# Optimization experiments

Measured on AMD Instinct MI355X. Metric: run time of the kernel, lower is better.

The kernel has to match this reference:

```python
import jax, jax.numpy as jnp
import numpy as np

EPS = 1e-5
INV_SQRT2 = 0.7071067811865476

def _rmsnorm(x, w):
    rms = jnp.sqrt(jnp.sum(x * x, axis=-1) / x.shape[-1] + EPS)
    return x / rms[..., None] * w

def _gelu(x):
    # exact erf-based GELU as in the torch module
    return x * (1.0 + jax.scipy.special.erf(x * INV_SQRT2)) * 0.5

def setup_inputs() -> dict:
    key = jax.random.key(0)
    ks = jax.random.split(key, 8)
    B, S, D, DFF = 4, 2048, 1024, 4096
    s = 0.02  # realistic init scale keeps softmax non-degenerate
    return {
        "x": jax.random.normal(ks[0], (B, S, D), jnp.float32),
        "ln1": jax.random.uniform(ks[1], (D,), jnp.float32),
        "ln2": jax.random.uniform(ks[2], (D,), jnp.float32),
        "ffn1": jax.random.normal(ks[3], (DFF, D), jnp.float32) * s,
        "ffn2": jax.random.normal(ks[4], (D, DFF), jnp.float32) * s,
        "k_proj": jax.random.normal(ks[5], (D, D), jnp.float32) * s,
        "q_proj": jax.random.normal(ks[6], (D, D), jnp.float32) * s,
        "v_proj": jax.random.normal(ks[7], (D, D), jnp.float32) * s,
        "out_proj": jax.random.normal(jax.random.fold_in(key, 99), (D, D), jnp.float32) * s,
    }

def reference(x, ln1, ln2, ffn1, ffn2, k_proj, q_proj, v_proj, out_proj):
    S = x.shape[1]
    d_k = x.shape[-1]
    # --- attention branch (single-head, as in source) ---
    h = _rmsnorm(x, ln1)
    Q = h @ q_proj.T  # [B,S,D]
    K = h @ k_proj.T
    V = h @ v_proj.T
    scores = jnp.einsum('bqd,bkd->bqk', Q, K) / jnp.sqrt(jnp.float32(d_k))
    attn = jax.nn.softmax(scores, axis=-1)
    # source: softmax first, then zero out strict-upper (future) entries, renormalize
    causal = jnp.tril(jnp.ones((S, S), jnp.float32))
    attn = attn * causal
    attn = attn / jnp.sum(attn, axis=-1, keepdims=True)
    mh = jnp.einsum('bqk,bkd->bqd', attn, V) @ out_proj
    y = x + mh
    # --- FFN branch: NOTE source feeds RMSNorm2(x), not y ---
    h2 = _rmsnorm(x, ln2)
    ff = _gelu(h2 @ ffn1.T) @ ffn2.T
    return y + ff
```

## Files before the change

kernel.cpp:

```cpp
#include <hip/hip_runtime.h>
#include <math.h>

typedef __bf16 bf16_t;
typedef __bf16 bf16x8 __attribute__((ext_vector_type(8)));
typedef float f32x4 __attribute__((ext_vector_type(4)));

#define LDS16(g, l) __builtin_amdgcn_global_load_lds( \
    (__attribute__((address_space(1))) void*)(g),     \
    (__attribute__((address_space(3))) void*)(l), 16, 0, 0)

__global__ __launch_bounds__(256) void prep_kernel(
    const float* __restrict__ qp, const float* __restrict__ kp,
    const float* __restrict__ vp, const float* __restrict__ f1,
    const float* __restrict__ f2, const float* __restrict__ op,
    const float* __restrict__ x, const float* __restrict__ ln1,
    bf16_t* __restrict__ qkvb, bf16_t* __restrict__ f1b,
    bf16_t* __restrict__ f2b, bf16_t* __restrict__ opT,
    bf16_t* __restrict__ h1)
{
    __shared__ float tile[32][33];
    __shared__ float red[4];
    int bid = blockIdx.x;
    int t = threadIdx.x;
    if (bid < 11264) {
        size_t i = ((size_t)bid * 256 + t) * 4;
        const float* src;
        bf16_t* dst;
        if (i < 3145728) {
            if (i < 1048576)      { src = qp + i;             dst = qkvb + i; }
            else if (i < 2097152) { src = kp + (i - 1048576); dst = qkvb + i; }
            else                  { src = vp + (i - 2097152); dst = qkvb + i; }
        } else if (i < 7340032) { src = f1 + (i - 3145728); dst = f1b + (i - 3145728); }
        else                    { src = f2 + (i - 7340032); dst = f2b + (i - 7340032); }
        float4 v = *(const float4*)src;
        dst[0] = (bf16_t)v.x; dst[1] = (bf16_t)v.y;
        dst[2] = (bf16_t)v.z; dst[3] = (bf16_t)v.w;
    } else if (bid < 12288) {
        int b2 = bid - 11264;
        int c0 = (b2 & 31) * 32, r0 = (b2 >> 5) * 32;
        int tx = t & 31, ty = t >> 5;
#pragma unroll
        for (int i = 0; i < 32; i += 8)
            tile[ty + i][tx] = op[(size_t)(r0 + ty + i) * 1024 + c0 + tx];
        __syncthreads();
#pragma unroll
        for (int i = 0; i < 32; i += 8)
            opT[(size_t)(c0 + ty + i) * 1024 + r0 + tx] = (bf16_t)tile[tx][ty + i];
    } else {
        int row = bid - 12288;
        float4 xv = ((const float4*)(x + (size_t)row * 1024))[t];
        float ss = xv.x * xv.x + xv.y * xv.y + xv.z * xv.z + xv.w * xv.w;
#pragma unroll
        for (int o = 32; o > 0; o >>= 1) ss += __shfl_xor(ss, o, 64);
        if ((t & 63) == 0) red[t >> 6] = ss;
        __syncthreads();
        ss = red[0] + red[1] + red[2] + red[3];
        float rinv = rsqrtf(ss * (1.0f / 1024.0f) + 1e-5f);
        float4 wv = ((const float4*)ln1)[t];
        bf16_t* hp = h1 + (size_t)row * 1024 + t * 4;
        hp[0] = (bf16_t)(xv.x * rinv * wv.x);
        hp[1] = (bf16_t)(xv.y * rinv * wv.y);
        hp[2] = (bf16_t)(xv.z * rinv * wv.z);
        hp[3] = (bf16_t)(xv.w * rinv * wv.w);
    }
}

__global__ __launch_bounds__(256) void rmsnorm_kernel(
    const float* __restrict__ x, const float* __restrict__ w,
    bf16_t* __restrict__ h)
{
    int row = blockIdx.x;
    int t = threadIdx.x;
    float4 xv = ((const float4*)(x + (size_t)row * 1024))[t];
    float ss = xv.x * xv.x + xv.y * xv.y + xv.z * xv.z + xv.w * xv.w;
#pragma unroll
    for (int o = 32; o > 0; o >>= 1) ss += __shfl_xor(ss, o, 64);
    __shared__ float red[4];
    if ((t & 63) == 0) red[t >> 6] = ss;
    __syncthreads();
    ss = red[0] + red[1] + red[2] + red[3];
    float rinv = rsqrtf(ss * (1.0f / 1024.0f) + 1e-5f);
    float4 wv = ((const float4*)w)[t];
    bf16_t* hp = h + (size_t)row * 1024 + t * 4;
    hp[0] = (bf16_t)(xv.x * rinv * wv.x);
    hp[1] = (bf16_t)(xv.y * rinv * wv.y);
    hp[2] = (bf16_t)(xv.z * rinv * wv.z);
    hp[3] = (bf16_t)(xv.w * rinv * wv.w);
}

__global__ __launch_bounds__(256) void transpose_bf16(
    const bf16_t* __restrict__ in, bf16_t* __restrict__ out,
    int rows, int ldin, long long sIn, long long sOut)
{
    __shared__ bf16_t tile[32][33];
    int b = blockIdx.z;
    const bf16_t* ip = in + (long long)b * sIn;
    bf16_t* op = out + (long long)b * sOut;
    int c0 = blockIdx.x * 32, r0 = blockIdx.y * 32;
    int tx = threadIdx.x & 31, ty = threadIdx.x >> 5;
#pragma unroll
    for (int i = 0; i < 32; i += 8)
        tile[ty + i][tx] = ip[(size_t)(r0 + ty + i) * ldin + c0 + tx];
    __syncthreads();
#pragma unroll
    for (int i = 0; i < 32; i += 8)
        op[(size_t)(c0 + ty + i) * rows + r0 + tx] = tile[tx][ty + i];
}

__global__ __launch_bounds__(256) void causal_softmax_kernel(bf16_t* __restrict__ SP)
{
    const int S = 2048;
    int q = blockIdx.x, b = blockIdx.y;
    bf16_t* row = SP + ((size_t)b * S + q) * S;
    int t = threadIdx.x;
    int j0 = t * 8;
    int Jstore = ((q >> 7) + 1) << 7;

    float v[8];
    if (j0 + 7 <= q) {
        bf16x8 xv = *(const bf16x8*)(row + j0);
#pragma unroll
        for (int i = 0; i < 8; i++) v[i] = (float)xv[i];
    } else if (j0 <= q) {
#pragma unroll
        for (int i = 0; i < 8; i++)
            v[i] = (j0 + i <= q) ? (float)row[j0 + i] : -1e30f;
    } else {
#pragma unroll
        for (int i = 0; i < 8; i++) v[i] = -1e30f;
    }

    float mx = v[0];
#pragma unroll
    for (int i = 1; i < 8; i++) mx = fmaxf(mx, v[i]);
#pragma unroll
    for (int o = 32; o > 0; o >>= 1) mx = fmaxf(mx, __shfl_xor(mx, o, 64));
    __shared__ float sm[4], ssum[4];
    if ((t & 63) == 0) sm[t >> 6] = mx;
    __syncthreads();
    mx = fmaxf(fmaxf(sm[0], sm[1]), fmaxf(sm[2], sm[3]));

    float e[8];
    float sum = 0.f;
#pragma unroll
    for (int i = 0; i < 8; i++) {
        e[i] = (v[i] > -1e29f) ? expf(v[i] - mx) : 0.f;
        sum += e[i];
    }
#pragma unroll
    for (int o = 32; o > 0; o >>= 1) sum += __shfl_xor(sum, o, 64);
    if ((t & 63) == 0) ssum[t >> 6] = sum;
    __syncthreads();
    sum = ssum[0] + ssum[1] + ssum[2] + ssum[3];
    float r = 1.0f / sum;

    if (j0 < Jstore) {
        bf16x8 ov;
#pragma unroll
        for (int i = 0; i < 8; i++) ov[i] = (bf16_t)(e[i] * r);
        *(bf16x8*)(row + j0) = ov;
    }
}

template <int EPI, bool CSKIP, bool CKLOOP, bool ASPLIT>
__global__ __launch_bounds__(256) void gemm_bt(
    const bf16_t* __restrict__ A, const bf16_t* __restrict__ A2, int lda,
    const bf16_t* __restrict__ B, int ldb,
    void* Cv, int ldc, const float* R,
    int K, int Ksp, int Mt, long long sA, long long sB, long long sC,
    float scale)
{
    int id = blockIdx.x, bz = blockIdx.z;
    int xcd = id & 7, p = id >> 3;
    int chunk = Mt >> 3;
    int bm = xcd * chunk + (p % chunk);
    int bn = p / chunk;
    if (CSKIP && bn > bm) return;

    __shared__ __align__(16) bf16_t At[128 * 64];
    __shared__ __align__(16) bf16_t Bt[128 * 64];
    int t = threadIdx.x;
    int w = t >> 6, l = t & 63;
    int wm = w >> 1, wn = w & 1;
    int lane_m = l & 15, quad = l >> 4;

    const bf16_t* Ag = A + (long long)bz * sA + (size_t)(bm * 128) * lda;
    const bf16_t* Bg = B + (long long)bz * sB + (size_t)(bn * 128) * ldb;

    int Keff = K;
    if (CKLOOP) {
        int kk = (bm + 1) * 128;
        if (kk < K) Keff = kk;
    }

    f32x4 acc[4][4] = {};

    int rb = w * 8 + (l >> 3);
    int g0 = ((l & 7) ^ ((l >> 3) & 7)) * 8;
    const bf16_t* a0[4];
    const bf16_t* a1[4];
    const bf16_t* b0[4];
#pragma unroll
    for (int j = 0; j < 4; j++) {
        size_t ro = (size_t)(rb + 32 * j);
        a0[j] = Ag + ro * lda + g0;
        if (ASPLIT) a1[j] = A2 + (long long)bz * sA + (size_t)(bm * 128) * lda
                           + ro * lda + g0;
        b0[j] = Bg + ro * ldb + g0;
    }

    int s0 = (quad ^ (lane_m & 7)) * 8;
    int s1 = ((4 + quad) ^ (lane_m & 7)) * 8;

    for (int kt = 0; kt < Keff; kt += 64) {
        __syncthreads();
#pragma unroll
        for (int j = 0; j < 4; j++) {
            const bf16_t* pa = a0[j] + kt;
            if (ASPLIT && kt >= Ksp) pa = a1[j] + (kt - Ksp);
            LDS16(pa, At + (size_t)w * 512 + j * 2048);
            LDS16(b0[j] + kt, Bt + (size_t)w * 512 + j * 2048);
        }
        __syncthreads();

#pragma unroll
        for (int h = 0; h < 2; h++) {
            int sh = h ? s1 : s0;
            bf16x8 af[4], bfr[4];
#pragma unroll
            for (int mi = 0; mi < 4; mi++)
                af[mi] = *(const bf16x8*)(At + (wm * 64 + mi * 16 + lane_m) * 64 + sh);
#pragma unroll
            for (int ni = 0; ni < 4; ni++)
                bfr[ni] = *(const bf16x8*)(Bt + (wn * 64 + ni * 16 + lane_m) * 64 + sh);
#pragma unroll
            for (int mi = 0; mi < 4; mi++)
#pragma unroll
                for (int ni = 0; ni < 4; ni++)
                    acc[mi][ni] = __builtin_amdgcn_mfma_f32_16x16x32_bf16(
                        af[mi], bfr[ni], acc[mi][ni], 0, 0, 0);
        }
    }

    long long cbase = (long long)bz * sC;
#pragma unroll
    for (int mi = 0; mi < 4; mi++) {
#pragma unroll
        for (int r = 0; r < 4; r++) {
            int row = bm * 128 + wm * 64 + mi * 16 + quad * 4 + r;
#pragma unroll
            for (int ni = 0; ni < 4; ni++) {
                int col = bn * 128 + wn * 64 + ni * 16 + lane_m;
                float v = acc[mi][ni][r];
                size_t idx = (size_t)(cbase + (long long)row * ldc + col);
                if (EPI == 0) {
                    ((bf16_t*)Cv)[idx] = (bf16_t)(v * scale);
                } else if (EPI == 1) {
                    float g = 0.5f * v * (1.0f + erff(v * 0.70710678118654752f));
                    ((bf16_t*)Cv)[idx] = (bf16_t)g;
                } else {
                    float rv = R[(size_t)row * ldc + col];
                    ((float*)Cv)[idx] = v + rv;
                }
            }
        }
    }
}

template <int EPI>
__global__ __launch_bounds__(512, 2) void gemm8p(
    const bf16_t* __restrict__ A, int lda,
    const bf16_t* __restrict__ B, int ldb,
    void* Cv, int ldc, const float* R, int K, float scale)
{
    int id = blockIdx.x;
    int xcd = id & 7, p = id >> 3;
    int bm = xcd * 4 + (p & 3);
    int bn = p >> 2;

    __shared__ __align__(16) bf16_t As[2][256 * 64];
    __shared__ __align__(16) bf16_t Bs[2][128 * 64];

    int t = threadIdx.x;
    int w = t >> 6, l = t & 63;
    int wm = w >> 1, wn = w & 1;
    int lane_m = l & 15, quad = l >> 4;

    const bf16_t* Ag = A + (size_t)(bm * 256) * lda;
    const bf16_t* Bg = B + (size_t)(bn * 128) * ldb;

    int rsub = w * 8 + (l >> 3);
    int g0 = ((l & 7) ^ ((l >> 3) & 7)) * 8;
    const bf16_t* pA0 = Ag + (size_t)(rsub)       * lda + g0;
    const bf16_t* pA1 = Ag + (size_t)(64 + rsub)  * lda + g0;
    const bf16_t* pA2 = Ag + (size_t)(128 + rsub) * lda + g0;
    const bf16_t* pA3 = Ag + (size_t)(192 + rsub) * lda + g0;
    const bf16_t* pB0 = Bg + (size_t)(rsub)       * ldb + g0;
    const bf16_t* pB1 = Bg + (size_t)(64 + rsub)  * ldb + g0;

    int sl0 = (quad ^ (lane_m & 7)) * 8;
    int sl1 = ((4 + quad) ^ (lane_m & 7)) * 8;
    int arow = (wm * 64 + lane_m) * 64;
    int brow = (wn * 64 + lane_m) * 64;

    f32x4 acc[4][4] = {};

    LDS16(pA0, &As[0][0 * 4096 + w * 512]);
    LDS16(pA1, &As[0][1 * 4096 + w * 512]);
    LDS16(pA2, &As[0][2 * 4096 + w * 512]);
    LDS16(pA3, &As[0][3 * 4096 + w * 512]);
    LDS16(pB0, &Bs[0][0 * 4096 + w * 512]);
    LDS16(pB1, &Bs[0][1 * 4096 + w * 512]);
    asm volatile("s_waitcnt vmcnt(0)" ::: "memory");
    __builtin_amdgcn_s_barrier();

    int cur = 0;
    for (int kt = 0; kt < K; kt += 64) {
        const bool pf = (kt + 64) < K;
        const int nxt = cur ^ 1;
        const bf16_t* Ac = As[cur];
        const bf16_t* Bc = Bs[cur];
        bf16x8 af[2], bfr0[4], bfr1[4];

        af[0] = *(const bf16x8*)(Ac + arow + 0 * 1024 + sl0);
        af[1] = *(const bf16x8*)(Ac + arow + 1 * 1024 + sl0);
#pragma unroll
        for (int ni = 0; ni < 4; ni++)
            bfr0[ni] = *(const bf16x8*)(Bc + brow + ni * 1024 + sl0);
        if (pf) {
            LDS16(pA0 + kt + 64, &As[nxt][0 * 4096 + w * 512]);
            LDS16(pA1 + kt + 64, &As[nxt][1 * 4096 + w * 512]);
            LDS16(pA2 + kt + 64, &As[nxt][2 * 4096 + w * 512]);
            LDS16(pA3 + kt + 64, &As[nxt][3 * 4096 + w * 512]);
        }
        __builtin_amdgcn_s_barrier();
        asm volatile("s_waitcnt lgkmcnt(0)" ::: "memory");
        __builtin_amdgcn_sched_barrier(0);
        __builtin_amdgcn_s_setprio(1);
#pragma unroll
        for (int j = 0; j < 2; j++)
#pragma unroll
            for (int ni = 0; ni < 4; ni++)
                acc[j][ni] = __builtin_amdgcn_mfma_f32_16x16x32_bf16(
                    af[j], bfr0[ni], acc[j][ni], 0, 0, 0);
        __builtin_amdgcn_s_setprio(0);
        __builtin_amdgcn_s_barrier();

        af[0] = *(const bf16x8*)(Ac + arow + 0 * 1024 + sl1);
        af[1] = *(const bf16x8*)(Ac + arow + 1 * 1024 + sl1);
#pragma unroll
        for (int ni = 0; ni < 4; ni++)
            bfr1[ni] = *(const bf16x8*)(Bc + brow + ni * 1024 + sl1);
        if (pf) {
            LDS16(pB0 + kt + 64, &Bs[nxt][0 * 4096 + w * 512]);
            LDS16(pB1 + kt + 64, &Bs[nxt][1 * 4096 + w * 512]);
        }
        __builtin_amdgcn_s_barrier();
        asm volatile("s_waitcnt lgkmcnt(0)" ::: "memory");
        __builtin_amdgcn_sched_barrier(0);
        __builtin_amdgcn_s_setprio(1);
#pragma unroll
        for (int j = 0; j < 2; j++)
#pragma unroll
            for (int ni = 0; ni < 4; ni++)
                acc[j][ni] = __builtin_amdgcn_mfma_f32_16x16x32_bf16(
                    af[j], bfr1[ni], acc[j][ni], 0, 0, 0);
        __builtin_amdgcn_s_setprio(0);
        __builtin_amdgcn_s_barrier();

        af[0] = *(const bf16x8*)(Ac + arow + 2 * 1024 + sl0);
        af[1] = *(const bf16x8*)(Ac + arow + 3 * 1024 + sl0);
        __builtin_amdgcn_s_barrier();
        asm volatile("s_waitcnt lgkmcnt(0)" ::: "memory");
        __builtin_amdgcn_sched_barrier(0);
        __builtin_amdgcn_s_setprio(1);
#pragma unroll
        for (int j = 0; j < 2; j++)
#pragma unroll
            for (int ni = 0; ni < 4; ni++)
                acc[2 + j][ni] = __builtin_amdgcn_mfma_f32_16x16x32_bf16(
                    af[j], bfr0[ni], acc[2 + j][ni], 0, 0, 0);
        __builtin_amdgcn_s_setprio(0);
        __builtin_amdgcn_s_barrier();

        af[0] = *(const bf16x8*)(Ac + arow + 2 * 1024 + sl1);
        af[1] = *(const bf16x8*)(Ac + arow + 3 * 1024 + sl1);
        __builtin_amdgcn_s_barrier();
        asm volatile("s_waitcnt lgkmcnt(0)" ::: "memory");
        __builtin_amdgcn_sched_barrier(0);
        __builtin_amdgcn_s_setprio(1);
#pragma unroll
        for (int j = 0; j < 2; j++)
#pragma unroll
            for (int ni = 0; ni < 4; ni++)
                acc[2 + j][ni] = __builtin_amdgcn_mfma_f32_16x16x32_bf16(
                    af[j], bfr1[ni], acc[2 + j][ni], 0, 0, 0);
        __builtin_amdgcn_s_setprio(0);
        if (pf) asm volatile("s_waitcnt vmcnt(0)" ::: "memory");
        __builtin_amdgcn_s_barrier();

        cur = nxt;
    }

#pragma unroll
    for (int mi = 0; mi < 4; mi++) {
#pragma unroll
        for (int r = 0; r < 4; r++) {
            int row = bm * 256 + wm * 64 + mi * 16 + quad * 4 + r;
#pragma unroll
            for (int ni = 0; ni < 4; ni++) {
                int col = bn * 128 + wn * 64 + ni * 16 + lane_m;
                float v = acc[mi][ni][r];
                size_t idx = (size_t)row * ldc + col;
                if (EPI == 0) {
                    ((bf16_t*)Cv)[idx] = (bf16_t)(v * scale);
                } else if (EPI == 1) {
                    float g = 0.5f * v * (1.0f + erff(v * 0.70710678118654752f));
                    ((bf16_t*)Cv)[idx] = (bf16_t)g;
                } else {
                    float rv = R[(size_t)row * ldc + col];
                    ((float*)Cv)[idx] = v + rv;
                }
            }
        }
    }
}

extern "C" void kernel_launch(void* const* d_in, const int* in_sizes, int n_in,
                              void* d_out, int out_size, void* d_ws, size_t ws_size,
                              hipStream_t stream)
{
    (void)in_sizes; (void)n_in; (void)out_size;
    const float* x    = (const float*)d_in[0];
    const float* ln1  = (const float*)d_in[1];
    const float* ln2  = (const float*)d_in[2];
    const float* ffn1 = (const float*)d_in[3];
    const float* ffn2 = (const float*)d_in[4];
    const float* kp   = (const float*)d_in[5];
    const float* qp   = (const float*)d_in[6];
    const float* vp   = (const float*)d_in[7];
    const float* op   = (const float*)d_in[8];
    float* out = (float*)d_out;

    const size_t MiB = 1048576;
    char* ws = (char*)d_ws;
    bf16_t* qkvb = (bf16_t*)(ws + 0 * MiB);
    bf16_t* opT  = (bf16_t*)(ws + 6 * MiB);
    bf16_t* f1b  = (bf16_t*)(ws + 8 * MiB);
    bf16_t* f2b  = (bf16_t*)(ws + 16 * MiB);
    bf16_t* h1   = (bf16_t*)(ws + 24 * MiB);
    bf16_t* VT   = (bf16_t*)(ws + 24 * MiB);
    bf16_t* h2   = (bf16_t*)(ws + 24 * MiB);
    bf16_t* QKVb = (bf16_t*)(ws + 40 * MiB);
    bf16_t* AV   = (bf16_t*)(ws + 40 * MiB);
    bf16_t* G0   = (bf16_t*)(ws + 40 * MiB);
    bf16_t* SP   = (bf16_t*)d_out;
    bool bigws = ws_size >= 104 * MiB;

    dim3 blk(256);
    dim3 blk8(512);
    const int HUGE_K = 1 << 30;

    prep_kernel<<<dim3(20480), blk, 0, stream>>>(
        qp, kp, vp, ffn1, ffn2, op, x, ln1, qkvb, f1b, f2b, opT, h1);

    gemm8p<0><<<dim3(768), blk8, 0, stream>>>(
        h1, 1024, qkvb, 1024, QKVb, 3072, nullptr, 1024, 1.0f);

    gemm_bt<0, true, false, false><<<dim3(256, 1, 4), blk, 0, stream>>>(
        QKVb, QKVb, 3072, QKVb + 1024, 3072, SP, 2048, nullptr,
        1024, HUGE_K, 16,
        (long long)2048 * 3072, (long long)2048 * 3072, (long long)2048 * 2048,
        1.0f / 32.0f);

    transpose_bf16<<<dim3(32, 64, 4), blk, 0, stream>>>(
        QKVb + 2048, VT, 2048, 3072,
        (long long)2048 * 3072, (long long)1024 * 2048);

    causal_softmax_kernel<<<dim3(2048, 4), blk, 0, stream>>>(SP);

    gemm_bt<0, false, true, false><<<dim3(128, 1, 4), blk, 0, stream>>>(
        SP, SP, 2048, VT, 2048, AV, 1024, nullptr,
        2048, HUGE_K, 16,
        (long long)2048 * 2048, (long long)1024 * 2048, (long long)2048 * 1024,
        1.0f);

    gemm8p<2><<<dim3(256), blk8, 0, stream>>>(
        AV, 1024, opT, 1024, out, 1024, x, 1024, 1.0f);

    rmsnorm_kernel<<<dim3(8192), blk, 0, stream>>>(x, ln2, h2);

    if (bigws) {
        gemm8p<1><<<dim3(1024), blk8, 0, stream>>>(
            h2, 1024, f1b, 1024, G0, 4096, nullptr, 1024, 1.0f);
        gemm8p<2><<<dim3(256), blk8, 0, stream>>>(
            G0, 4096, f2b, 4096, out, 1024, out, 4096, 1.0f);
    } else {
        for (int half = 0; half < 2; half++) {
            gemm_bt<1, false, false, false><<<dim3(1024), blk, 0, stream>>>(
                h2, h2, 1024, f1b + (size_t)half * 2048 * 1024, 1024, G0, 2048,
                nullptr, 1024, HUGE_K, 64, 0, 0, 0, 1.0f);
            gemm_bt<2, false, false, false><<<dim3(512), blk, 0, stream>>>(
                G0, G0, 2048, f2b + half * 2048, 4096, out, 1024, out,
                2048, HUGE_K, 64, 0, 0, 0, 1.0f);
        }
    }
}
```

Before: 542.9 us.

## Triple-buffer LDS tiles in gemm8p to prefetch two K-steps ahead

```diff
diff --git a/kernel.cpp b/kernel.cpp
--- a/kernel.cpp
+++ b/kernel.cpp
@@ -278,8 +278,8 @@
     int bm = xcd * 4 + (p & 3);
     int bn = p >> 2;
 
-    __shared__ __align__(16) bf16_t As[2][256 * 64];
-    __shared__ __align__(16) bf16_t Bs[2][128 * 64];
+    __shared__ __align__(16) bf16_t As[3][256 * 64];
+    __shared__ __align__(16) bf16_t Bs[3][128 * 64];
 
     int t = threadIdx.x;
     int w = t >> 6, l = t & 63;
@@ -311,13 +311,24 @@
     LDS16(pA3, &As[0][3 * 4096 + w * 512]);
     LDS16(pB0, &Bs[0][0 * 4096 + w * 512]);
     LDS16(pB1, &Bs[0][1 * 4096 + w * 512]);
-    asm volatile("s_waitcnt vmcnt(0)" ::: "memory");
+    if (64 < K) {
+        LDS16(pA0 + 64, &As[1][0 * 4096 + w * 512]);
+        LDS16(pA1 + 64, &As[1][1 * 4096 + w * 512]);
+        LDS16(pA2 + 64, &As[1][2 * 4096 + w * 512]);
+        LDS16(pA3 + 64, &As[1][3 * 4096 + w * 512]);
+        LDS16(pB0 + 64, &Bs[1][0 * 4096 + w * 512]);
+        LDS16(pB1 + 64, &Bs[1][1 * 4096 + w * 512]);
+        asm volatile("s_waitcnt vmcnt(6)" ::: "memory");
+    } else {
+        asm volatile("s_waitcnt vmcnt(0)" ::: "memory");
+    }
     __builtin_amdgcn_s_barrier();
 
     int cur = 0;
     for (int kt = 0; kt < K; kt += 64) {
-        const bool pf = (kt + 64) < K;
-        const int nxt = cur ^ 1;
+        const bool pf2 = (kt + 128) < K;
+        int nxt = cur + 1; if (nxt >= 3) nxt -= 3;
+        int nn  = cur + 2; if (nn  >= 3) nn  -= 3;
         const bf16_t* Ac = As[cur];
         const bf16_t* Bc = Bs[cur];
         bf16x8 af[2], bfr0[4], bfr1[4];
@@ -327,11 +338,11 @@
 #pragma unroll
         for (int ni = 0; ni < 4; ni++)
             bfr0[ni] = *(const bf16x8*)(Bc + brow + ni * 1024 + sl0);
-        if (pf) {
-            LDS16(pA0 + kt + 64, &As[nxt][0 * 4096 + w * 512]);
-            LDS16(pA1 + kt + 64, &As[nxt][1 * 4096 + w * 512]);
-            LDS16(pA2 + kt + 64, &As[nxt][2 * 4096 + w * 512]);
-            LDS16(pA3 + kt + 64, &As[nxt][3 * 4096 + w * 512]);
+        if (pf2) {
+            LDS16(pA0 + kt + 128, &As[nn][0 * 4096 + w * 512]);
+            LDS16(pA1 + kt + 128, &As[nn][1 * 4096 + w * 512]);
+            LDS16(pA2 + kt + 128, &As[nn][2 * 4096 + w * 512]);
+            LDS16(pA3 + kt + 128, &As[nn][3 * 4096 + w * 512]);
         }
         __builtin_amdgcn_s_barrier();
         asm volatile("s_waitcnt lgkmcnt(0)" ::: "memory");
@@ -351,9 +362,9 @@
 #pragma unroll
         for (int ni = 0; ni < 4; ni++)
             bfr1[ni] = *(const bf16x8*)(Bc + brow + ni * 1024 + sl1);
-        if (pf) {
-            LDS16(pB0 + kt + 64, &Bs[nxt][0 * 4096 + w * 512]);
-            LDS16(pB1 + kt + 64, &Bs[nxt][1 * 4096 + w * 512]);
+        if (pf2) {
+            LDS16(pB0 + kt + 128, &Bs[nn][0 * 4096 + w * 512]);
+            LDS16(pB1 + kt + 128, &Bs[nn][1 * 4096 + w * 512]);
         }
         __builtin_amdgcn_s_barrier();
         asm volatile("s_waitcnt lgkmcnt(0)" ::: "memory");
@@ -396,7 +407,8 @@
                 acc[2 + j][ni] = __builtin_amdgcn_mfma_f32_16x16x32_bf16(
                     af[j], bfr1[ni], acc[2 + j][ni], 0, 0, 0);
         __builtin_amdgcn_s_setprio(0);
-        if (pf) asm volatile("s_waitcnt vmcnt(0)" ::: "memory");
+        if (pf2) asm volatile("s_waitcnt vmcnt(6)" ::: "memory");
+        else     asm volatile("s_waitcnt vmcnt(0)" ::: "memory");
         __builtin_amdgcn_s_barrier();
 
         cur = nxt;
```

Measured after the change: 546.6 us. No clear change (+0.7%).
